# Kernel tuning notes

Hardware: AMD Instinct MI355X
Metric: run time of the kernel (lower is better)

## Reference

```python
import jax, jax.numpy as jnp
import numpy as np

B, T, I, H = 4, 512, 128, 128


def _lstm(x, Wih, Whh, b):
    """Standard LSTM (PyTorch gate order i,f,g,o). x: [B,T,I] -> h: [B,T,H]."""
    xg = jnp.swapaxes(x, 0, 1) @ Wih.T + b  # [T,B,4H] input projections precomputed
    Hh = Whh.shape[1]
    h0 = jnp.zeros((x.shape[0], Hh), x.dtype)
    c0 = jnp.zeros((x.shape[0], Hh), x.dtype)

    def step(carry, xg_t):
        h, c = carry
        g = xg_t + h @ Whh.T
        i, f, gg, o = jnp.split(g, 4, axis=-1)
        c = jax.nn.sigmoid(f) * c + jax.nn.sigmoid(i) * jnp.tanh(gg)
        h = jax.nn.sigmoid(o) * jnp.tanh(c)
        return (h, c), h

    _, hs = jax.lax.scan(step, (h0, c0), xg)
    return jnp.swapaxes(hs, 0, 1)  # [B,T,H]


def setup_inputs() -> dict:
    key = jax.random.key(0)
    ks = jax.random.split(key, 12)
    s = 0.1
    return {
        "x": jax.random.normal(ks[0], (B, T, I), jnp.float32),
        # shared LSTM
        "Wih_s": jax.random.normal(ks[1], (4 * H, I), jnp.float32) * s,
        "Whh_s": jax.random.normal(ks[2], (4 * H, H), jnp.float32) * s,
        "b_lstm_s": jnp.zeros((4 * H,), jnp.float32),
        # Ws split along its concatenated input [x_sub; h_t; h_sub]
        "Wx": jax.random.normal(ks[3], (I, H), jnp.float32) * s,
        "Wht": jax.random.normal(ks[4], (H, H), jnp.float32) * s,
        "Whs": jax.random.normal(ks[5], (H, H), jnp.float32) * s,
        "bs": jnp.zeros((H,), jnp.float32),
        # Us: H -> 1
        "u": jax.random.normal(ks[6], (H,), jnp.float32) * s,
        "bu": jnp.zeros((), jnp.float32),
        # task LSTM over [x; R] (input_size + hidden_size)
        "Wih_t": jax.random.normal(ks[7], (4 * H, I + H), jnp.float32) * s,
        "Whh_t": jax.random.normal(ks[8], (4 * H, H), jnp.float32) * s,
        "b_lstm_t": jnp.zeros((4 * H,), jnp.float32),
    }


def reference(x, Wih_s, Whh_s, b_lstm_s, Wx, Wht, Whs, bs, u, bu,
              Wih_t, Whh_t, b_lstm_t):
    # 1) shared LSTM encoding
    Hsh = _lstm(x, Wih_s, Whh_s, b_lstm_s)  # [B,T,H]

    # 2) pairwise attention scores S[b,t,s] = Us(tanh(Ws([x_s; h_t; h_s])))
    #    decompose Ws over its concatenated input to avoid building the concat
    xp = x @ Wx          # [B,T,H] (indexed by s)
    hp_t = Hsh @ Wht     # [B,T,H] (indexed by t)
    hp_s = Hsh @ Whs     # [B,T,H] (indexed by s)
    # M[b,t,s,:]: [B,T,T,H] — the dominant (memory-bound) intermediate
    M = jnp.tanh(hp_t[:, :, None, :] + (xp + hp_s)[:, None, :, :] + bs)
    scores = jnp.einsum("btsh,h->bts", M, u) + bu  # [B,T,T]

    # 3) softmax over sub_t and weighted sum of shared outputs
    beta = jax.nn.softmax(scores, axis=-1)         # [B,T,T]
    R = jnp.einsum("bts,bsh->bth", beta, Hsh)      # [B,T,H]

    # 4) task-specific LSTM consuming the input and the aggregated message
    h_task = _lstm(jnp.concatenate([x, R], axis=-1), Wih_t, Whh_t, b_lstm_t)
    return h_task  # [B,T,H]
```

## Files before the change

kernel.cpp:

```cpp
#include <hip/hip_runtime.h>
#include <hip/hip_bf16.h>
#include <math.h>

#define Bq 4
#define Tq 512
#define Hq 128

typedef _Float16 f16x4 __attribute__((ext_vector_type(4)));
typedef _Float16 f16x8 __attribute__((ext_vector_type(8)));
typedef float f32x4 __attribute__((ext_vector_type(4)));

__device__ __forceinline__ float rcp_fast(float x) { return __builtin_amdgcn_rcpf(x); }
__device__ __forceinline__ float sigmoid_fast(float x) {
    return rcp_fast(1.0f + __expf(-x));
}
__device__ __forceinline__ float tanh_fast(float x) {
    float e = __expf(2.0f * x);
    return 1.0f - 2.0f * rcp_fast(e + 1.0f);
}

__device__ __forceinline__ void gemm_nt_body(float (*As)[68], float (*Ws)[68],
                                             const float* __restrict__ A, int lda,
                                             const float* __restrict__ W, int ldw,
                                             const float* __restrict__ bias,
                                             float* __restrict__ C, int acc_flag,
                                             int m0, int n0, int tid) {
    int tx = tid & 15, ty = tid >> 4;
    float acc[4][4] = {};
    for (int kc = 0; kc < 2; kc++) {
        __syncthreads();
#pragma unroll
        for (int i = 0; i < 4; i++) {
            int idx = tid + 256 * i;
            int r = idx >> 4, c4 = idx & 15;
            *(float4*)(&As[r][c4 * 4]) = *(const float4*)(A + (size_t)(m0 + r) * lda + kc * 64 + c4 * 4);
            *(float4*)(&Ws[r][c4 * 4]) = *(const float4*)(W + (size_t)(n0 + r) * ldw + kc * 64 + c4 * 4);
        }
        __syncthreads();
#pragma unroll
        for (int k4 = 0; k4 < 16; k4++) {
            float4 a[4], wv[4];
#pragma unroll
            for (int i = 0; i < 4; i++) a[i] = *(const float4*)(&As[ty * 4 + i][k4 * 4]);
#pragma unroll
            for (int j = 0; j < 4; j++) wv[j] = *(const float4*)(&Ws[tx * 4 + j][k4 * 4]);
#pragma unroll
            for (int i = 0; i < 4; i++)
#pragma unroll
                for (int j = 0; j < 4; j++)
                    acc[i][j] += a[i].x * wv[j].x + a[i].y * wv[j].y + a[i].z * wv[j].z + a[i].w * wv[j].w;
        }
    }
#pragma unroll
    for (int i = 0; i < 4; i++) {
        int m = m0 + ty * 4 + i;
        int n = n0 + tx * 4;
        float4 v = make_float4(acc[i][0], acc[i][1], acc[i][2], acc[i][3]);
        if (bias) { v.x += bias[n]; v.y += bias[n + 1]; v.z += bias[n + 2]; v.w += bias[n + 3]; }
        if (acc_flag) {
            float4 o = *(const float4*)(C + (size_t)m * 512 + n);
            v.x += o.x; v.y += o.y; v.z += o.z; v.w += o.w;
        }
        *(float4*)(C + (size_t)m * 512 + n) = v;
    }
}

__device__ __forceinline__ void gemm_nt_512(float (*As)[68], float (*Ws)[68],
                                            const float* __restrict__ A, int lda,
                                            const float* __restrict__ W, int ldw,
                                            const float* __restrict__ bias,
                                            float* __restrict__ C,
                                            int m0, int n0, int tid) {
    int tx = tid & 15, ty = tid >> 4;
    float acc[2][4] = {};
    for (int kc = 0; kc < 2; kc++) {
        __syncthreads();
#pragma unroll
        for (int i = 0; i < 2; i++) {
            int idx = tid + 512 * i;
            int r = idx >> 4, c4 = idx & 15;
            *(float4*)(&As[r][c4 * 4]) = *(const float4*)(A + (size_t)(m0 + r) * lda + kc * 64 + c4 * 4);
            *(float4*)(&Ws[r][c4 * 4]) = *(const float4*)(W + (size_t)(n0 + r) * ldw + kc * 64 + c4 * 4);
        }
        __syncthreads();
#pragma unroll
        for (int k4 = 0; k4 < 16; k4++) {
            float4 a[2], wv[4];
#pragma unroll
            for (int i = 0; i < 2; i++) a[i] = *(const float4*)(&As[ty * 2 + i][k4 * 4]);
#pragma unroll
            for (int j = 0; j < 4; j++) wv[j] = *(const float4*)(&Ws[tx * 4 + j][k4 * 4]);
#pragma unroll
            for (int i = 0; i < 2; i++)
#pragma unroll
                for (int j = 0; j < 4; j++)
                    acc[i][j] += a[i].x * wv[j].x + a[i].y * wv[j].y + a[i].z * wv[j].z + a[i].w * wv[j].w;
        }
    }
#pragma unroll
    for (int i = 0; i < 2; i++) {
        int m = m0 + ty * 2 + i;
        int n = n0 + tx * 4;
        float4 v = make_float4(acc[i][0], acc[i][1], acc[i][2], acc[i][3]);
        if (bias) { v.x += bias[n]; v.y += bias[n + 1]; v.z += bias[n + 2]; v.w += bias[n + 3]; }
        *(float4*)(C + (size_t)m * 512 + n) = v;
    }
}

__global__ __launch_bounds__(256) void prep(const float* __restrict__ x,
                                            const float* __restrict__ Wih_s,
                                            const float* __restrict__ b_s,
                                            const float* __restrict__ Whh_s,
                                            float* __restrict__ xg_s,
                                            _Float16* __restrict__ W16_s) {
    __shared__ __align__(16) float As[64][68];
    __shared__ __align__(16) float Ws[64][68];
    int bid = blockIdx.x;
    int tid = threadIdx.x;
    if (bid < 256) {
        gemm_nt_body(As, Ws, x, 128, Wih_s, 128, b_s, xg_s, 0,
                     (bid & 31) * 64, (bid >> 5) * 64, tid);
    } else {
        int cb = bid - 256;
        int i = (cb * 256 + tid) * 4;
        float4 v = *(const float4*)(Whh_s + i);
        f16x4 o;
        o[0] = (_Float16)v.x; o[1] = (_Float16)v.y;
        o[2] = (_Float16)v.z; o[3] = (_Float16)v.w;
        *(f16x4*)(W16_s + i) = o;
    }
}

__global__ __launch_bounds__(256) void gemm_nt(const float* __restrict__ A, int lda,
                                               const float* __restrict__ W, int ldw,
                                               const float* __restrict__ bias,
                                               float* __restrict__ C, int acc_flag) {
    __shared__ __align__(16) float As[64][68];
    __shared__ __align__(16) float Ws[64][68];
    gemm_nt_body(As, Ws, A, lda, W, ldw, bias, C, acc_flag,
                 blockIdx.x * 64, blockIdx.y * 64, threadIdx.x);
}

__global__ __launch_bounds__(256) void mid(const float* __restrict__ x,
                                           const float* __restrict__ Hsh,
                                           const float* __restrict__ Wht,
                                           const float* __restrict__ Wx,
                                           const float* __restrict__ Whs,
                                           const float* __restrict__ bs,
                                           float* __restrict__ hp_t,
                                           float* __restrict__ c_sT) {
    __shared__ __align__(16) float As[64][68];
    __shared__ __align__(16) float Bs[64][68];
    int bid = blockIdx.x;
    int cfg = bid >> 6;
    int b2 = bid & 63;
    int m0 = (b2 & 31) * 64, n0 = (b2 >> 5) * 64;
    const float* A1 = cfg ? x : Hsh;
    const float* B1 = cfg ? Wx : Wht;
    const float* A2 = cfg ? Hsh : nullptr;
    const float* B2 = cfg ? Whs : nullptr;

    int tid = threadIdx.x;
    int tx = tid & 15, ty = tid >> 4;
    float acc[4][4] = {};
    for (int src = 0; src < 2; src++) {
        const float* A = src ? A2 : A1;
        const float* Bm = src ? B2 : B1;
        if (!A) break;
        for (int kc = 0; kc < 2; kc++) {
            __syncthreads();
#pragma unroll
            for (int i = 0; i < 4; i++) {
                int idx = tid + 256 * i;
                int r = idx >> 4, c4 = idx & 15;
                *(float4*)(&As[r][c4 * 4]) = *(const float4*)(A + (size_t)(m0 + r) * 128 + kc * 64 + c4 * 4);
                *(float4*)(&Bs[r][c4 * 4]) = *(const float4*)(Bm + (size_t)(kc * 64 + r) * 128 + n0 + c4 * 4);
            }
            __syncthreads();
#pragma unroll
            for (int k4 = 0; k4 < 16; k4++) {
                float4 a[4];
#pragma unroll
                for (int i = 0; i < 4; i++) a[i] = *(const float4*)(&As[ty * 4 + i][k4 * 4]);
#pragma unroll
                for (int kk = 0; kk < 4; kk++) {
                    float4 bv = *(const float4*)(&Bs[k4 * 4 + kk][tx * 4]);
#pragma unroll
                    for (int i = 0; i < 4; i++) {
                        float av = (kk == 0) ? a[i].x : (kk == 1) ? a[i].y : (kk == 2) ? a[i].z : a[i].w;
                        acc[i][0] += av * bv.x;
                        acc[i][1] += av * bv.y;
                        acc[i][2] += av * bv.z;
                        acc[i][3] += av * bv.w;
                    }
                }
            }
        }
    }
    if (cfg == 0) {
#pragma unroll
        for (int i = 0; i < 4; i++) {
            int m = m0 + ty * 4 + i;
            int n = n0 + tx * 4;
            *(float4*)(hp_t + (size_t)m * 128 + n) =
                make_float4(acc[i][0], acc[i][1], acc[i][2], acc[i][3]);
        }
    } else {
        __syncthreads();
#pragma unroll
        for (int i = 0; i < 4; i++)
#pragma unroll
            for (int j = 0; j < 4; j++)
                As[ty * 4 + i][tx * 4 + j] = acc[i][j] + bs[n0 + tx * 4 + j];
        __syncthreads();
        int b = m0 >> 9;
        int s0 = m0 & 511;
        int lane = tid & 63, wv = tid >> 6;
#pragma unroll 4
        for (int it = 0; it < 16; ++it) {
            int nl = wv * 16 + it;
            c_sT[((size_t)(b * 128 + n0 + nl)) * 512 + s0 + lane] = As[lane][nl];
        }
    }
}

#define MF0(ACC, A, B) \
    asm("v_mfma_f32_16x16x32_f16 %0, %1, %2, %3" : "=&v"(ACC) : "v"(A), "a"(B), "v"(zro));
#define MF(ACC, A, B) \
    asm("v_mfma_f32_16x16x32_f16 %0, %1, %2, %0" : "+v"(ACC) : "v"(A), "a"(B));

#define LSTM_STEP(X0, X1, X2, X3, R0, R1, R2, R3, WPTR, PXG)                       \
    {                                                                              \
        f16x8 a0 = *(R0); f16x8 a1 = *(R1);                                        \
        f16x8 a2 = *(R2); f16x8 a3 = *(R3);                                        \
        float o0 = X0, o1 = X1, o2 = X2, o3 = X3;                                  \
        X0 = (PXG)[0]; X1 = (PXG)[128]; X2 = (PXG)[256]; X3 = (PXG)[384];          \
        (PXG) += 1024;                                                             \
        f32x4 ac0a, ac1a, ac2a, ac3a, ac0b, ac1b, ac2b, ac3b;                      \
        MF0(ac0a, a0, b00) MF0(ac1a, a0, b10) MF0(ac2a, a0, b20) MF0(ac3a, a0, b30)\
        MF0(ac0b, a2, b02) MF0(ac1b, a2, b12) MF0(ac2b, a2, b22) MF0(ac3b, a2, b32)\
        MF(ac0a, a1, b01) MF(ac1a, a1, b11) MF(ac2a, a1, b21) MF(ac3a, a1, b31)    \
        MF(ac0b, a3, b03) MF(ac1b, a3, b13) MF(ac2b, a3, b23) MF(ac3b, a3, b33)    \
        __builtin_amdgcn_sched_barrier(0);                                         \
        asm volatile("s_nop 7\n\ts_nop 7"                                          \
                     :: "v"(ac0a), "v"(ac1a), "v"(ac2a), "v"(ac3a),                \
                        "v"(ac0b), "v"(ac1b), "v"(ac2b), "v"(ac3b));               \
        __builtin_amdgcn_sched_barrier(0);                                         \
        float gi = ac0a[0] + ac0b[0] + o0;                                         \
        float gf = ac1a[0] + ac1b[0] + o1;                                         \
        float gg = ac2a[0] + ac2b[0] + o2;                                         \
        float go = ac3a[0] + ac3b[0] + o3;                                         \
        float si = sigmoid_fast(gi), sf = sigmoid_fast(gf), so = sigmoid_fast(go); \
        float tg = tanh_fast(gg);                                                  \
        c = sf * c + si * tg;                                                      \
        float h = so * tanh_fast(c);                                               \
        *(WPTR) = (_Float16)h;                                                     \
        *pH = h; pH += Hq;                                                         \
        __builtin_amdgcn_sched_barrier(0);                                         \
        asm volatile("s_waitcnt lgkmcnt(0)");                                      \
        __builtin_amdgcn_s_barrier();                                              \
        __builtin_amdgcn_sched_barrier(0);                                         \
    }

__device__ __forceinline__ void lstm_core(const float* __restrict__ xg,
                                          const _Float16* __restrict__ W16,
                                          float* __restrict__ Hout,
                                          _Float16* hbase, int tid) {
    int w = tid >> 6, lane = tid & 63;
    int r = lane & 15, kg = lane >> 4;
    int ch = 16 * w + r;

    for (int i = tid; i < 4096; i += 512) hbase[i] = (_Float16)0.f;

    const _Float16* wb = W16 + (size_t)ch * 128 + kg * 8;
#define LWB(g, kb) *(const f16x8*)(wb + (size_t)(g) * 16384 + (kb) * 32)
    f16x8 b00 = LWB(0, 0), b01 = LWB(0, 1), b02 = LWB(0, 2), b03 = LWB(0, 3);
    f16x8 b10 = LWB(1, 0), b11 = LWB(1, 1), b12 = LWB(1, 2), b13 = LWB(1, 3);
    f16x8 b20 = LWB(2, 0), b21 = LWB(2, 1), b22 = LWB(2, 2), b23 = LWB(2, 3);
    f16x8 b30 = LWB(3, 0), b31 = LWB(3, 1), b32 = LWB(3, 2), b33 = LWB(3, 3);
#undef LWB
    f32x4 zro = {0.f, 0.f, 0.f, 0.f};
    asm volatile(""
                 : "+a"(b00), "+a"(b01), "+a"(b02), "+a"(b03),
                   "+a"(b10), "+a"(b11), "+a"(b12), "+a"(b13),
                   "+a"(b20), "+a"(b21), "+a"(b22), "+a"(b23),
                   "+a"(b30), "+a"(b31), "+a"(b32), "+a"(b33),
                   "+v"(zro));

    int aoff0 = r * 128 + (((0 * 4 + kg) ^ r) << 3);
    int aoff1 = r * 128 + (((1 * 4 + kg) ^ r) << 3);
    int aoff2 = r * 128 + (((2 * 4 + kg) ^ r) << 3);
    int aoff3 = r * 128 + (((3 * 4 + kg) ^ r) << 3);
    int woff = (4 * kg) * 128 + (((ch >> 3) ^ (4 * kg)) << 3) + (ch & 7);

    const f16x8* rA0 = (const f16x8*)(hbase + aoff0);
    const f16x8* rA1 = (const f16x8*)(hbase + aoff1);
    const f16x8* rA2 = (const f16x8*)(hbase + aoff2);
    const f16x8* rA3 = (const f16x8*)(hbase + aoff3);
    const f16x8* rB0 = (const f16x8*)(hbase + 2048 + aoff0);
    const f16x8* rB1 = (const f16x8*)(hbase + 2048 + aoff1);
    const f16x8* rB2 = (const f16x8*)(hbase + 2048 + aoff2);
    const f16x8* rB3 = (const f16x8*)(hbase + 2048 + aoff3);
    _Float16* wA = hbase + 2048 + woff;
    _Float16* wB = hbase + woff;

    size_t kgTq = (size_t)kg * Tq;
    const float* p0 = xg + (kgTq + 0) * 512 + ch;
    const float* p1 = xg + (kgTq + 1) * 512 + ch;
    float xa0 = p0[0], xa1 = p0[128], xa2 = p0[256], xa3 = p0[384];
    float xb0 = p1[0], xb1 = p1[128], xb2 = p1[256], xb3 = p1[384];
    const float* pA = xg + (kgTq + 2) * 512 + ch;
    const float* pB = xg + (kgTq + 3) * 512 + ch;
    float* pH = Hout + kgTq * Hq + ch;

    float c = 0.f;
    __syncthreads();

    for (int t = 0; t < Tq; t += 2) {
        LSTM_STEP(xa0, xa1, xa2, xa3, rA0, rA1, rA2, rA3, wA, pA)
        LSTM_STEP(xb0, xb1, xb2, xb3, rB0, rB1, rB2, rB3, wB, pB)
    }
}

__global__ __launch_bounds__(512)
__attribute__((amdgpu_waves_per_eu(2, 2)))
void lstm_fused(const float* __restrict__ xg_s,
                const _Float16* __restrict__ W16_s,
                float* __restrict__ Hsh,
                const float* __restrict__ x,
                const float* __restrict__ Wih_t,
                const float* __restrict__ b_t,
                const float* __restrict__ Whh_t,
                float* __restrict__ xg_t,
                _Float16* __restrict__ W16_t) {
    __shared__ __align__(16) float smem[2][64][68];
    int bid = blockIdx.x;
    int tid = threadIdx.x;
    if (bid == 0) {
        lstm_core(xg_s, W16_s, Hsh, (_Float16*)&smem[0][0][0], tid);
    } else if (bid <= 256) {
        int b2 = bid - 1;
        gemm_nt_512(smem[0], smem[1], x, 128, Wih_t, 256, b_t, xg_t,
                    (b2 & 31) * 64, (b2 >> 5) * 64, tid);
    } else {
        int cb = bid - 257;
        int i = (cb * 512 + tid) * 2;
        float2 v = *(const float2*)(Whh_t + i);
        W16_t[i] = (_Float16)v.x;
        W16_t[i + 1] = (_Float16)v.y;
    }
}

__global__ __launch_bounds__(512)
__attribute__((amdgpu_waves_per_eu(2, 2)))
void lstm_b4(const float* __restrict__ xg,
             const _Float16* __restrict__ W16,
             float* __restrict__ Hout) {
    __shared__ _Float16 hbuf[2][16][128];
    lstm_core(xg, W16, Hout, &hbuf[0][0][0], threadIdx.x);
}

__global__ __launch_bounds__(256) void attn_kernel(const float* __restrict__ hp_t,
                                                   const float* __restrict__ c_sT,
                                                   const float* __restrict__ u,
                                                   const float* __restrict__ Hsh,
                                                   float* __restrict__ R) {
    int t = blockIdx.x, b = blockIdx.y;
    int tid = threadIdx.x;
    __shared__ __align__(16) float a2_lds[128];
    __shared__ __align__(16) float un2_lds[128];
    __shared__ __align__(16) float sc[512];
    __shared__ __align__(16) float red[256];

    if (tid < 128) {
        a2_lds[tid] = 2.0f * hp_t[((size_t)b * Tq + t) * Hq + tid];
        un2_lds[tid] = -2.0f * u[tid];
    }
    __syncthreads();

    const float* pc = c_sT + (size_t)b * 65536 + tid;
    float acc0 = 0.f, acc1 = 0.f;
#pragma unroll 4
    for (int h = 0; h < 128; ++h) {
        float c0 = pc[0];
        float c1 = pc[256];
        float a2 = a2_lds[h], un2 = un2_lds[h];
        float e0 = __expf(fmaf(2.0f, c0, a2));
        float e1 = __expf(fmaf(2.0f, c1, a2));
        acc0 = fmaf(un2, rcp_fast(e0 + 1.0f), acc0);
        acc1 = fmaf(un2, rcp_fast(e1 + 1.0f), acc1);
        pc += 512;
    }
    float p0 = __expf(acc0), p1 = __expf(acc1);
    sc[tid] = p0;
    sc[tid + 256] = p1;

    float psum = p0 + p1;
#pragma unroll
    for (int off = 1; off < 64; off <<= 1) psum += __shfl_xor(psum, off, 64);
    int lane = tid & 63, wv = tid >> 6;
    if (lane == 0) red[wv] = psum;
    __syncthreads();
    float rinv = rcp_fast(red[0] + red[1] + red[2] + red[3]);

    int h = tid & 127, half = tid >> 7;
    float acc = 0.0f;
    for (int s = half; s < 512; s += 2) {
        acc += sc[s] * Hsh[((size_t)b * Tq + s) * Hq + h];
    }
    red[tid] = acc;
    __syncthreads();
    if (tid < 128) {
        R[((size_t)b * Tq + t) * Hq + tid] = (red[tid] + red[tid + 128]) * rinv;
    }
}

extern "C" void kernel_launch(void* const* d_in, const int* in_sizes, int n_in,
                              void* d_out, int out_size, void* d_ws, size_t ws_size,
                              hipStream_t stream) {
    const float* x      = (const float*)d_in[0];
    const float* Wih_s  = (const float*)d_in[1];
    const float* Whh_s  = (const float*)d_in[2];
    const float* b_s    = (const float*)d_in[3];
    const float* Wx     = (const float*)d_in[4];
    const float* Wht    = (const float*)d_in[5];
    const float* Whs    = (const float*)d_in[6];
    const float* bs     = (const float*)d_in[7];
    const float* u      = (const float*)d_in[8];
    const float* Wih_t  = (const float*)d_in[10];
    const float* Whh_t  = (const float*)d_in[11];
    const float* b_t    = (const float*)d_in[12];
    float* out = (float*)d_out;

    float* ws    = (float*)d_ws;
    float* xg_s  = ws;
    float* xg_t  = ws + 1048576;
    float* Hsh   = ws + 2097152;
    float* hp_t  = ws + 2359296;
    float* c_sT  = ws + 2621440;
    float* Rbuf  = ws + 2883584;
    _Float16* W16_t = (_Float16*)(ws + 3145728);
    _Float16* W16_s = (_Float16*)hp_t;

    dim3 blk(256);

    prep<<<320, blk, 0, stream>>>(x, Wih_s, b_s, Whh_s, xg_s, W16_s);

    lstm_fused<<<321, 512, 0, stream>>>(xg_s, W16_s, Hsh,
                                        x, Wih_t, b_t, Whh_t, xg_t, W16_t);

    mid<<<128, blk, 0, stream>>>(x, Hsh, Wht, Wx, Whs, bs, hp_t, c_sT);

    attn_kernel<<<dim3(Tq, Bq), blk, 0, stream>>>(hp_t, c_sT, u, Hsh, Rbuf);

    gemm_nt<<<dim3(32, 8), blk, 0, stream>>>(Rbuf, 128, Wih_t + 128, 256, nullptr, xg_t, 1);

    lstm_b4<<<1, 512, 0, stream>>>(xg_t, W16_t, out);
}
```

Before: 615.5 us.

## Process four query rows per attention block with vectorized score loads

The attention kernel now handles four t rows per 512-thread block instead of one row per 256-thread block. Each thread computes four consecutive s scores using float4 loads of c_sT, and the weighted sum over Hsh runs per query row without a cross-half reduction. The aim is to share c_sT and Hsh traffic across rows through cache locality, widen loads, and cut block count and sync overhead. In exchange, per-thread register use rises and the block count drops to 512, which lowers parallelism.

```diff
diff --git a/kernel.cpp b/kernel.cpp
--- a/kernel.cpp
+++ b/kernel.cpp
@@ -360,59 +360,62 @@
     lstm_core(xg, W16, Hout, &hbuf[0][0][0], threadIdx.x);
 }
 
-__global__ __launch_bounds__(256) void attn_kernel(const float* __restrict__ hp_t,
+__global__ __launch_bounds__(512) void attn_kernel(const float* __restrict__ hp_t,
                                                    const float* __restrict__ c_sT,
                                                    const float* __restrict__ u,
                                                    const float* __restrict__ Hsh,
                                                    float* __restrict__ R) {
-    int t = blockIdx.x, b = blockIdx.y;
+    int t0 = blockIdx.x * 4;
+    int b = blockIdx.y;
     int tid = threadIdx.x;
-    __shared__ __align__(16) float a2_lds[128];
+    int tq = tid >> 7, th = tid & 127;
+
+    __shared__ __align__(16) float a2_lds[4][128];
     __shared__ __align__(16) float un2_lds[128];
-    __shared__ __align__(16) float sc[512];
-    __shared__ __align__(16) float red[256];
-
-    if (tid < 128) {
-        a2_lds[tid] = 2.0f * hp_t[((size_t)b * Tq + t) * Hq + tid];
-        un2_lds[tid] = -2.0f * u[tid];
-    }
+    __shared__ __align__(16) float sc[4][512];
+    __shared__ __align__(16) float red[8];
+
+    a2_lds[tq][th] = 2.0f * hp_t[((size_t)b * Tq + t0 + tq) * Hq + th];
+    if (tid < 128) un2_lds[tid] = -2.0f * u[tid];
     __syncthreads();
 
-    const float* pc = c_sT + (size_t)b * 65536 + tid;
-    float acc0 = 0.f, acc1 = 0.f;
+    const float* pc = c_sT + (size_t)b * 65536 + 4 * th;
+    const float* pa = &a2_lds[tq][0];
+    float acc0 = 0.f, acc1 = 0.f, acc2 = 0.f, acc3 = 0.f;
 #pragma unroll 4
     for (int h = 0; h < 128; ++h) {
-        float c0 = pc[0];
-        float c1 = pc[256];
-        float a2 = a2_lds[h], un2 = un2_lds[h];
-        float e0 = __expf(fmaf(2.0f, c0, a2));
-        float e1 = __expf(fmaf(2.0f, c1, a2));
+        float4 cv = *(const float4*)pc;
+        float a2 = pa[h], un2 = un2_lds[h];
+        float e0 = __expf(fmaf(2.0f, cv.x, a2));
+        float e1 = __expf(fmaf(2.0f, cv.y, a2));
+        float e2 = __expf(fmaf(2.0f, cv.z, a2));
+        float e3 = __expf(fmaf(2.0f, cv.w, a2));
         acc0 = fmaf(un2, rcp_fast(e0 + 1.0f), acc0);
         acc1 = fmaf(un2, rcp_fast(e1 + 1.0f), acc1);
+        acc2 = fmaf(un2, rcp_fast(e2 + 1.0f), acc2);
+        acc3 = fmaf(un2, rcp_fast(e3 + 1.0f), acc3);
         pc += 512;
     }
     float p0 = __expf(acc0), p1 = __expf(acc1);
-    sc[tid] = p0;
-    sc[tid + 256] = p1;
-
-    float psum = p0 + p1;
+    float p2 = __expf(acc2), p3 = __expf(acc3);
+    *(float4*)&sc[tq][4 * th] = make_float4(p0, p1, p2, p3);
+
+    float psum = p0 + p1 + p2 + p3;
 #pragma unroll
     for (int off = 1; off < 64; off <<= 1) psum += __shfl_xor(psum, off, 64);
-    int lane = tid & 63, wv = tid >> 6;
-    if (lane == 0) red[wv] = psum;
+    int wv = tid >> 6;
+    if ((tid & 63) == 0) red[wv] = psum;
     __syncthreads();
-    float rinv = rcp_fast(red[0] + red[1] + red[2] + red[3]);
-
-    int h = tid & 127, half = tid >> 7;
+    float rinv = rcp_fast(red[2 * tq] + red[2 * tq + 1]);
+
+    const float* hb = Hsh + (size_t)b * Tq * Hq + th;
+    const float* scp = &sc[tq][0];
     float acc = 0.0f;
-    for (int s = half; s < 512; s += 2) {
-        acc += sc[s] * Hsh[((size_t)b * Tq + s) * Hq + h];
-    }
-    red[tid] = acc;
-    __syncthreads();
-    if (tid < 128) {
-        R[((size_t)b * Tq + t) * Hq + tid] = (red[tid] + red[tid + 128]) * rinv;
-    }
+#pragma unroll 4
+    for (int s = 0; s < 512; ++s) {
+        acc = fmaf(scp[s], hb[(size_t)s * Hq], acc);
+    }
+    R[((size_t)b * Tq + t0 + tq) * Hq + th] = acc * rinv;
 }
 
 extern "C" void kernel_launch(void* const* d_in, const int* in_sizes, int n_in,
@@ -451,7 +454,7 @@
 
     mid<<<128, blk, 0, stream>>>(x, Hsh, Wht, Wx, Whs, bs, hp_t, c_sT);
 
-    attn_kernel<<<dim3(Tq, Bq), blk, 0, stream>>>(hp_t, c_sT, u, Hsh, Rbuf);
+    attn_kernel<<<dim3(Tq / 4, Bq), 512, 0, stream>>>(hp_t, c_sT, u, Hsh, Rbuf);
 
     gemm_nt<<<dim3(32, 8), blk, 0, stream>>>(Rbuf, 128, Wih_t + 128, 256, nullptr, xg_t, 1);
 
```

New measurement: 584.8 us. 5.0% less time.
